# Performance work log

Hardware: AMD Instinct MI355X
Metric: run time of the kernel (lower is better)

## Reference

```python
import jax, jax.numpy as jnp
import numpy as np

GROUPS = 32
EPS = 1e-5

def group_norm(x, scale, bias):
    b, c, h, w = x.shape
    xg = x.reshape(b, GROUPS, c // GROUPS, h, w)
    mean = xg.mean(axis=(2, 3, 4), keepdims=True)
    var = xg.var(axis=(2, 3, 4), keepdims=True)
    xg = (xg - mean) * jax.lax.rsqrt(var + EPS)
    x = xg.reshape(b, c, h, w)
    return x * scale[None, :, None, None] + bias[None, :, None, None]

def conv2d(x, w, b, pad):
    y = jax.lax.conv_general_dilated(
        x, w, window_strides=(1, 1), padding=[(pad, pad), (pad, pad)],
        dimension_numbers=('NCHW', 'OIHW', 'NCHW'))
    return y + b[None, :, None, None]

def setup_inputs() -> dict:
    key = jax.random.key(0)
    ks = jax.random.split(key, 16)
    B, Cin, Cout, H, W, TDIM, NCON = 4, 128, 128, 64, 64, 512, 4
    s = 0.05
    return {
        'x': jax.random.normal(ks[0], (B, Cin, H, W), jnp.float32),
        't': jax.random.normal(ks[1], (B, TDIM), jnp.float32),
        'aim': jax.random.randint(ks[2], (B,), 0, NCON),
        'cond': jax.random.normal(ks[3], (B, Cin, H, W), jnp.float32),
        'gn1_scale': jnp.ones((Cin,), jnp.float32),
        'gn1_bias': jnp.zeros((Cin,), jnp.float32),
        'conv1_w': jax.random.normal(ks[4], (Cout, Cin, 3, 3), jnp.float32) * s,
        'conv1_b': jnp.zeros((Cout,), jnp.float32),
        'mlp_w': jax.random.normal(ks[5], (Cout, TDIM), jnp.float32) * s,
        'mlp_b': jnp.zeros((Cout,), jnp.float32),
        'cond_w': jax.random.normal(ks[6], (Cout, Cin, 1, 1), jnp.float32) * s,
        'cond_b': jnp.zeros((Cout,), jnp.float32),
        'gn2_scale': jnp.ones((Cout,), jnp.float32),
        'gn2_bias': jnp.zeros((Cout,), jnp.float32),
        'conv2_w': jax.random.normal(ks[7], (Cout, Cout, 3, 3), jnp.float32) * s,
        'conv2_b': jnp.zeros((Cout,), jnp.float32),
        'contrast_embed': jax.random.normal(ks[8], (NCON, Cout, 1, 1), jnp.float32),
    }

def reference(x, t, aim, cond, gn1_scale, gn1_bias, conv1_w, conv1_b,
              mlp_w, mlp_b, cond_w, cond_b, gn2_scale, gn2_bias,
              conv2_w, conv2_b, contrast_embed):
    # block1: GN -> SiLU -> 3x3 conv
    h = conv2d(jax.nn.silu(group_norm(x, gn1_scale, gn1_bias)), conv1_w, conv1_b, 1)
    # time embedding: SiLU -> Linear, broadcast over spatial
    temb = jax.nn.silu(t) @ mlp_w.T + mlp_b  # (b, out_ch)
    h = h + temb[:, :, None, None]
    # spatial cross-attention with cond
    c = conv2d(cond, cond_w, cond_b, 0)  # 1x1 projection, (b, C, u, v)
    C = h.shape[1]
    score = jnp.einsum('bchw,bcuv->bhwuv', h, c)  # (b, h, w, u, v)
    # NOTE: softmax over dim=1 (the spatial h axis), as in the source
    score = jax.nn.softmax(score / jnp.sqrt(jnp.float32(C)), axis=1)
    h = h + jnp.einsum('bhwuv,bcuv->bchw', score, c)
    # contrast embedding lookup
    h = h + contrast_embed[aim]  # (b, C, 1, 1) broadcast
    # block2: GN -> SiLU -> (dropout=identity at eval) -> 3x3 conv
    h = conv2d(jax.nn.silu(group_norm(h, gn2_scale, gn2_bias)), conv2_w, conv2_b, 1)
    # res_conv is Identity since in_ch == out_ch
    return h + x
```

## Files before the change

### kernel.cpp

```cpp
#include <hip/hip_runtime.h>
#include <cmath>

#define BB 4
#define CC 128
#define HH 64
#define WW 64
#define SP 4096
#define NG 32
#define TT 64
#define NS 4
#define PSZ ((size_t)BB * SP * CC)

typedef __bf16 bf16x8 __attribute__((ext_vector_type(8)));
typedef __bf16 bf16x4 __attribute__((ext_vector_type(4)));
typedef float  f32x4  __attribute__((ext_vector_type(4)));

__device__ __forceinline__ float silu_f(float v) {
    return v / (1.f + __expf(-v));
}

__global__ __launch_bounds__(256) void prep_kernel(
    const float* __restrict__ x, const float* __restrict__ gn1s,
    const float* __restrict__ gn1b, __bf16* __restrict__ aT,
    const float* __restrict__ c1w, const float* __restrict__ c2w,
    __bf16* __restrict__ wt,
    const float* __restrict__ t, const float* __restrict__ mlpw,
    const float* __restrict__ mlpb, float* __restrict__ tembw,
    const float* __restrict__ cond, const float* __restrict__ cw,
    const float* __restrict__ cb, __bf16* __restrict__ cmT,
    __bf16* __restrict__ cm2)
{
    __shared__ __align__(16) char pool[65536];
    __shared__ float rs[4], rs2[4], mean_s, inv_s;
    const int blk = blockIdx.x;
    const int tid = threadIdx.x;

    if (blk < 128) {
        const int b = blk >> 5, g = blk & 31;
        float* X = (float*)pool;
        const float* p = x + (size_t)blk * 16384;
        float s = 0.f, s2 = 0.f;
        for (int it = 0; it < 16; ++it) {
            int q = it * 256 + tid;
            float4 v = *(const float4*)&p[q * 4];
            *(float4*)&X[q * 4] = v;
            s += v.x + v.y + v.z + v.w;
            s2 += v.x * v.x + v.y * v.y + v.z * v.z + v.w * v.w;
        }
        #pragma unroll
        for (int off = 32; off >= 1; off >>= 1) {
            s  += __shfl_down(s,  off, 64);
            s2 += __shfl_down(s2, off, 64);
        }
        const int wid = tid >> 6;
        if ((tid & 63) == 0) { rs[wid] = s; rs2[wid] = s2; }
        __syncthreads();
        if (tid == 0) {
            float S = rs[0] + rs[1] + rs[2] + rs[3];
            float S2 = rs2[0] + rs2[1] + rs2[2] + rs2[3];
            float m = S * (1.f / 16384.f);
            float var = S2 * (1.f / 16384.f) - m * m;
            mean_s = m;
            inv_s = rsqrtf(var + 1e-5f);
        }
        __syncthreads();
        const float m = mean_s, inv = inv_s;
        float sc[4], bi[4];
        #pragma unroll
        for (int j = 0; j < 4; ++j) { sc[j] = gn1s[g * 4 + j]; bi[j] = gn1b[g * 4 + j]; }
        for (int it = 0; it < 16; ++it) {
            int pp = it * 256 + tid;
            bf16x4 o;
            #pragma unroll
            for (int j = 0; j < 4; ++j)
                o[j] = (__bf16)silu_f((X[j * 4096 + pp] - m) * inv * sc[j] + bi[j]);
            *(bf16x4*)&aT[((size_t)(b * SP + pp)) * CC + g * 4] = o;
        }
    } else if (blk < 146) {
        const int idx = blk - 128;
        const int wsel = idx / 9, tap = idx % 9;
        const float* src = wsel ? c2w : c1w;
        __bf16* dst = wt + (size_t)wsel * 9 * 16384 + (size_t)tap * 16384;
        for (int it = 0; it < 64; ++it) {
            int q = it * 256 + tid;
            dst[q] = (__bf16)src[(size_t)q * 9 + tap];
        }
    } else if (blk < 154) {
        const int cog = blk - 146;
        float* st = (float*)pool;
        float* wr = (float*)(pool + 8192);
        for (int it = 0; it < 8; ++it) {
            int q = it * 256 + tid;
            st[q] = silu_f(t[q]);
        }
        for (int it = 0; it < 8; ++it) {
            int q = it * 256 + tid;
            int row = q >> 7, col4 = q & 127;
            *(float4*)&wr[row * 512 + col4 * 4] =
                *(const float4*)&mlpw[(size_t)(cog * 16 + row) * 512 + col4 * 4];
        }
        __syncthreads();
        const int col = tid >> 4, seg = tid & 15;
        float acc[4] = {0.f, 0.f, 0.f, 0.f};
        for (int k = seg * 32; k < seg * 32 + 32; ++k) {
            float wv = wr[col * 512 + k];
            acc[0] += st[0 * 512 + k] * wv;
            acc[1] += st[1 * 512 + k] * wv;
            acc[2] += st[2 * 512 + k] * wv;
            acc[3] += st[3 * 512 + k] * wv;
        }
        #pragma unroll
        for (int o = 1; o < 16; o <<= 1) {
            #pragma unroll
            for (int b4 = 0; b4 < 4; ++b4)
                acc[b4] += __shfl_xor(acc[b4], o, 64);
        }
        if (seg == 0) {
            float bv = mlpb[cog * 16 + col];
            #pragma unroll
            for (int b4 = 0; b4 < 4; ++b4)
                tembw[b4 * 128 + cog * 16 + col] = acc[b4] + bv;
        }
    } else {
        const int pblk = blk - 154;
        const int b = pblk >> 6;
        const int p0 = (pblk & 63) * 64;
        const int l = tid & 63, wv = tid >> 6;
        const int l15 = l & 15, l4 = l >> 4;
        const int mB = wv * 32;

        __bf16* XT = (__bf16*)pool;
        __bf16* wl = (__bf16*)(pool + 17152);

        for (int it = 0; it < 32; ++it) {
            int q = it * 256 + tid;
            float v = cond[((size_t)(b * CC + (q >> 6))) * SP + p0 + (q & 63)];
            XT[(q & 63) * 134 + (q >> 6)] = (__bf16)v;
        }
        for (int it = 0; it < 64; ++it) {
            int q = it * 256 + tid;
            wl[(q >> 7) * 134 + (q & 127)] = (__bf16)cw[q];
        }
        __syncthreads();

        f32x4 acc[2][4];
        #pragma unroll
        for (int mb = 0; mb < 2; ++mb)
            #pragma unroll
            for (int nt = 0; nt < 4; ++nt) acc[mb][nt] = (f32x4){0.f, 0.f, 0.f, 0.f};

        #pragma unroll
        for (int ks = 0; ks < 4; ++ks) {
            bf16x8 bfr[4];
            #pragma unroll
            for (int nt = 0; nt < 4; ++nt)
                bfr[nt] = *(const bf16x8*)&XT[(nt * 16 + l15) * 134 + ks * 32 + l4 * 8];
            #pragma unroll
            for (int mb = 0; mb < 2; ++mb) {
                bf16x8 afr = *(const bf16x8*)&wl[(mB + mb * 16 + l15) * 134 + ks * 32 + l4 * 8];
                #pragma unroll
                for (int nt = 0; nt < 4; ++nt)
                    acc[mb][nt] = __builtin_amdgcn_mfma_f32_16x16x32_bf16(afr, bfr[nt], acc[mb][nt], 0, 0, 0);
            }
        }

        const float scl = 0.088388347648318447f;
        #pragma unroll
        for (int mb = 0; mb < 2; ++mb) {
            int co0 = mB + mb * 16 + l4 * 4;
            float bv[4];
            #pragma unroll
            for (int r = 0; r < 4; ++r) bv[r] = cb[co0 + r];
            #pragma unroll
            for (int nt = 0; nt < 4; ++nt) {
                int p = p0 + nt * 16 + l15;
                bf16x4 o;
                #pragma unroll
                for (int r = 0; r < 4; ++r)
                    o[r] = (__bf16)((acc[mb][nt][r] + bv[r]) * scl);
                *(bf16x4*)&cmT[((size_t)(b * SP + p)) * CC + co0] = o;
            }
        }
        __syncthreads();
        __bf16* O2 = wl;
        #pragma unroll
        for (int mb = 0; mb < 2; ++mb) {
            int co0 = mB + mb * 16 + l4 * 4;
            #pragma unroll
            for (int r = 0; r < 4; ++r) {
                float bv = cb[co0 + r];
                #pragma unroll
                for (int nt = 0; nt < 4; ++nt)
                    O2[(co0 + r) * 72 + nt * 16 + l15] = (__bf16)(acc[mb][nt][r] + bv);
            }
        }
        __syncthreads();
        #pragma unroll
        for (int it = 0; it < 4; ++it) {
            int q = it * 256 + tid;
            int co = q >> 3, pc = q & 7;
            *(bf16x8*)&cm2[((size_t)(b * CC + co)) * SP + p0 + pc * 8] =
                *(const bf16x8*)&O2[co * 72 + pc * 8];
        }
    }
}

template<bool FUSE_TEMB, bool OUT_CF>
__global__ __launch_bounds__(256, 3) void conv_mfma_kernel(
    const __bf16* __restrict__ inT, const __bf16* __restrict__ wt,
    const float* __restrict__ bias, const float* __restrict__ temb,
    const float* __restrict__ resid, __bf16* __restrict__ outT,
    float* __restrict__ outF)
{
    const int y   = blockIdx.x >> 1;
    const int coh = blockIdx.x & 1;
    const int b   = blockIdx.y;
    const int tid = threadIdx.x;
    const int l = tid & 63, wv = tid >> 6;
    const int l15 = l & 15, l4 = l >> 4;
    const int mB = (wv & 1) * 32;
    const int xh = (wv >> 1) * 32;

    __shared__ __bf16 inS[3 * 66 * 136];

    const __bf16* inTb = inT + (size_t)b * SP * CC;
    for (int q = tid; q < 3 * 66 * 16; q += 256) {
        int cc = q & 15;
        int xs = (q >> 4) % 66;
        int r  = (q >> 4) / 66;
        int yy = y + r - 1;
        int xg = xs - 1;
        bf16x8 v;
        if (((unsigned)yy < 64u) && ((unsigned)xg < 64u)) {
            v = *(const bf16x8*)&inTb[((size_t)(yy * 64 + xg)) * CC + cc * 8];
        } else {
            #pragma unroll
            for (int j = 0; j < 8; ++j) v[j] = (__bf16)0.f;
        }
        *(bf16x8*)&inS[(r * 66 + xs) * 136 + cc * 8] = v;
    }
    __syncthreads();

    f32x4 acc[2][2];
    #pragma unroll
    for (int mb = 0; mb < 2; ++mb)
        #pragma unroll
        for (int nb = 0; nb < 2; ++nb) acc[mb][nb] = (f32x4){0.f, 0.f, 0.f, 0.f};

    const __bf16* wp0 = wt + (size_t)(coh * 64 + mB + l15) * 128 + l4 * 8;
    const __bf16* wp1 = wt + (size_t)(coh * 64 + mB + 16 + l15) * 128 + l4 * 8;

    bf16x8 wb[2][2][4];
    #pragma unroll
    for (int ks = 0; ks < 4; ++ks) {
        wb[0][0][ks] = *(const bf16x8*)(wp0 + ks * 32);
        wb[0][1][ks] = *(const bf16x8*)(wp1 + ks * 32);
    }

    #pragma unroll
    for (int tap = 0; tap < 9; ++tap) {
        const int cur = tap & 1, nxt = cur ^ 1;
        if (tap < 8) {
            #pragma unroll
            for (int ks = 0; ks < 4; ++ks) {
                wb[nxt][0][ks] = *(const bf16x8*)(wp0 + (tap + 1) * 16384 + ks * 32);
                wb[nxt][1][ks] = *(const bf16x8*)(wp1 + (tap + 1) * 16384 + ks * 32);
            }
        }
        const __bf16* rb = &inS[((tap / 3) * 66 + xh + (tap % 3)) * 136];
        #pragma unroll
        for (int ks = 0; ks < 4; ++ks) {
            bf16x8 b0 = *(const bf16x8*)&rb[(l15) * 136 + ks * 32 + l4 * 8];
            bf16x8 b1 = *(const bf16x8*)&rb[(16 + l15) * 136 + ks * 32 + l4 * 8];
            acc[0][0] = __builtin_amdgcn_mfma_f32_16x16x32_bf16(wb[cur][0][ks], b0, acc[0][0], 0, 0, 0);
            acc[1][0] = __builtin_amdgcn_mfma_f32_16x16x32_bf16(wb[cur][1][ks], b0, acc[1][0], 0, 0, 0);
            acc[0][1] = __builtin_amdgcn_mfma_f32_16x16x32_bf16(wb[cur][0][ks], b1, acc[0][1], 0, 0, 0);
            acc[1][1] = __builtin_amdgcn_mfma_f32_16x16x32_bf16(wb[cur][1][ks], b1, acc[1][1], 0, 0, 0);
        }
    }

    if (OUT_CF) {
        #pragma unroll
        for (int mb = 0; mb < 2; ++mb) {
            #pragma unroll
            for (int r = 0; r < 4; ++r) {
                int co = coh * 64 + mB + mb * 16 + l4 * 4 + r;
                float bv = bias[co];
                #pragma unroll
                for (int nb = 0; nb < 2; ++nb) {
                    int p = y * 64 + xh + nb * 16 + l15;
                    size_t o = ((size_t)(b * CC + co)) * SP + p;
                    outF[o] = acc[mb][nb][r] + bv + resid[o];
                }
            }
        }
    } else {
        #pragma unroll
        for (int mb = 0; mb < 2; ++mb) {
            int co0 = coh * 64 + mB + mb * 16 + l4 * 4;
            float bv[4];
            #pragma unroll
            for (int r = 0; r < 4; ++r)
                bv[r] = bias[co0 + r] + (FUSE_TEMB ? temb[b * CC + co0 + r] : 0.f);
            #pragma unroll
            for (int nb = 0; nb < 2; ++nb) {
                int p = y * 64 + xh + nb * 16 + l15;
                bf16x4 o;
                #pragma unroll
                for (int r = 0; r < 4; ++r)
                    o[r] = (__bf16)(acc[mb][nb][r] + bv[r]);
                *(bf16x4*)&outT[((size_t)(b * SP + p)) * CC + co0] = o;
            }
        }
    }
}

#define CT2 72
#define PBS 72
#define POOL_BYTES 46080

__global__ __launch_bounds__(256, 3) void attn_kernel(
    const __bf16* __restrict__ h1T, const __bf16* __restrict__ cmT,
    const __bf16* __restrict__ cm2, __bf16* __restrict__ parts)
{
    const int w = blockIdx.x;
    const int b = blockIdx.y;
    const int s = blockIdx.z;
    const int tid = threadIdx.x;
    const int wl = tid >> 6;
    const int l = tid & 63, l15 = l & 15, l4 = l >> 4;
    const int hB = (wl & 1) * 32;
    const int cB = (wl >> 1) * 64;

    __shared__ __align__(16) char pool[POOL_BYTES];
    __bf16* ct2p = (__bf16*)pool;
    __bf16* Pb   = (__bf16*)(pool + 36864);
    __bf16* Otr  = (__bf16*)pool;

    const __bf16* h1Tb = h1T + (size_t)b * SP * CC;
    const __bf16* cmTb = cmT + (size_t)b * SP * CC;
    const __bf16* cm2b = cm2 + (size_t)b * CC * SP;

    bf16x8 hfr[4][4];
    #pragma unroll
    for (int nt = 0; nt < 4; ++nt)
        #pragma unroll
        for (int ks = 0; ks < 4; ++ks)
            hfr[nt][ks] = *(const bf16x8*)&h1Tb[((size_t)((nt * 16 + l15) * WW + w)) * CC + ks * 32 + l4 * 8];

    f32x4 acc2[2][4];
    #pragma unroll
    for (int mb = 0; mb < 2; ++mb)
        #pragma unroll
        for (int nt = 0; nt < 4; ++nt) acc2[mb][nt] = (f32x4){0.f, 0.f, 0.f, 0.f};

    const int sc = tid >> 3;
    const int stc = tid & 7;

    {
        const int uv0 = s * TT;
        #pragma unroll
        for (int it = 0; it < 4; ++it) {
            int c = it * 32 + sc;
            *(bf16x8*)&ct2p[c * CT2 + stc * 8] =
                *(const bf16x8*)&cm2b[(size_t)c * SP + uv0 + stc * 8];
        }
        const __bf16* arow = cmTb + (size_t)(uv0 + 16 * wl + l15) * CC;
        bf16x8 afr[4];
        #pragma unroll
        for (int ks = 0; ks < 4; ++ks) afr[ks] = *(const bf16x8*)&arow[ks * 32 + l4 * 8];
        f32x4 s1[4];
        #pragma unroll
        for (int nt = 0; nt < 4; ++nt) {
            s1[nt] = (f32x4){0.f, 0.f, 0.f, 0.f};
            #pragma unroll
            for (int ks = 0; ks < 4; ++ks)
                s1[nt] = __builtin_amdgcn_mfma_f32_16x16x32_bf16(afr[ks], hfr[nt][ks], s1[nt], 0, 0, 0);
        }
        #pragma unroll
        for (int r = 0; r < 4; ++r) {
            float e0 = __expf(s1[0][r]), e1 = __expf(s1[1][r]);
            float e2 = __expf(s1[2][r]), e3 = __expf(s1[3][r]);
            float sm = e0 + e1 + e2 + e3;
            sm += __shfl_xor(sm, 1, 64);
            sm += __shfl_xor(sm, 2, 64);
            sm += __shfl_xor(sm, 4, 64);
            sm += __shfl_xor(sm, 8, 64);
            float ri = 1.f / sm;
            s1[0][r] = e0 * ri; s1[1][r] = e1 * ri;
            s1[2][r] = e2 * ri; s1[3][r] = e3 * ri;
        }
        #pragma unroll
        for (int nt = 0; nt < 4; ++nt) {
            bf16x4 pk;
            pk[0] = (__bf16)s1[nt][0]; pk[1] = (__bf16)s1[nt][1];
            pk[2] = (__bf16)s1[nt][2]; pk[3] = (__bf16)s1[nt][3];
            *(bf16x4*)&Pb[(nt * 16 + l15) * PBS + 16 * wl + l4 * 4] = pk;
        }
    }

    for (int i = 0; i < SP / TT / NS; ++i) {
        const int cur = i & 1;
        __syncthreads();
        bf16x8 st4[4];
        bf16x8 afr[4];
        if (i < SP / TT / NS - 1) {
            const int uv0n = ((i + 1) * NS + s) * TT;
            #pragma unroll
            for (int it = 0; it < 4; ++it) {
                int c = it * 32 + sc;
                st4[it] = *(const bf16x8*)&cm2b[(size_t)c * SP + uv0n + stc * 8];
            }
            const __bf16* arow = cmTb + (size_t)(uv0n + 16 * wl + l15) * CC;
            #pragma unroll
            for (int ks = 0; ks < 4; ++ks) afr[ks] = *(const bf16x8*)&arow[ks * 32 + l4 * 8];
        }
        bf16x8 pfr[2][2];
        #pragma unroll
        for (int mb = 0; mb < 2; ++mb)
            #pragma unroll
            for (int ks = 0; ks < 2; ++ks)
                pfr[mb][ks] = *(const bf16x8*)&Pb[(hB + mb * 16 + l15) * PBS + ks * 32 + l4 * 8];
        __syncthreads();
        {
            const __bf16* ctR = ct2p + cur * 9216;
            #pragma unroll
            for (int mb = 0; mb < 2; ++mb)
                #pragma unroll
                for (int nt = 0; nt < 4; ++nt)
                    #pragma unroll
                    for (int ks = 0; ks < 2; ++ks) {
                        bf16x8 bfr = *(const bf16x8*)&ctR[(cB + nt * 16 + l15) * CT2 + ks * 32 + l4 * 8];
                        acc2[mb][nt] = __builtin_amdgcn_mfma_f32_16x16x32_bf16(
                            pfr[mb][ks], bfr, acc2[mb][nt], 0, 0, 0);
                    }
        }
        if (i < SP / TT / NS - 1) {
            __bf16* ctW = ct2p + (cur ^ 1) * 9216;
            #pragma unroll
            for (int it = 0; it < 4; ++it) {
                int c = it * 32 + sc;
                *(bf16x8*)&ctW[c * CT2 + stc * 8] = st4[it];
            }
            f32x4 s1[4];
            #pragma unroll
            for (int nt = 0; nt < 4; ++nt) {
                s1[nt] = (f32x4){0.f, 0.f, 0.f, 0.f};
                #pragma unroll
                for (int ks = 0; ks < 4; ++ks)
                    s1[nt] = __builtin_amdgcn_mfma_f32_16x16x32_bf16(afr[ks], hfr[nt][ks], s1[nt], 0, 0, 0);
            }
            #pragma unroll
            for (int r = 0; r < 4; ++r) {
                float e0 = __expf(s1[0][r]), e1 = __expf(s1[1][r]);
                float e2 = __expf(s1[2][r]), e3 = __expf(s1[3][r]);
                float sm = e0 + e1 + e2 + e3;
                sm += __shfl_xor(sm, 1, 64);
                sm += __shfl_xor(sm, 2, 64);
                sm += __shfl_xor(sm, 4, 64);
                sm += __shfl_xor(sm, 8, 64);
                float ri = 1.f / sm;
                s1[0][r] = e0 * ri; s1[1][r] = e1 * ri;
                s1[2][r] = e2 * ri; s1[3][r] = e3 * ri;
            }
            #pragma unroll
            for (int nt = 0; nt < 4; ++nt) {
                bf16x4 pk;
                pk[0] = (__bf16)s1[nt][0]; pk[1] = (__bf16)s1[nt][1];
                pk[2] = (__bf16)s1[nt][2]; pk[3] = (__bf16)s1[nt][3];
                *(bf16x4*)&Pb[(nt * 16 + l15) * PBS + 16 * wl + l4 * 4] = pk;
            }
        }
    }

    __syncthreads();
    #pragma unroll
    for (int mb = 0; mb < 2; ++mb)
        #pragma unroll
        for (int nt = 0; nt < 4; ++nt)
            #pragma unroll
            for (int r = 0; r < 4; ++r)
                Otr[(hB + mb * 16 + l4 * 4 + r) * 136 + cB + nt * 16 + l15] =
                    (__bf16)acc2[mb][nt][r];
    __syncthreads();
    __bf16* pO = parts + (size_t)s * PSZ;
    #pragma unroll
    for (int it = 0; it < 4; ++it) {
        int q = it * 256 + tid;
        int h = q >> 4, cc = q & 15;
        *(bf16x8*)&pO[((size_t)(b * SP + h * WW + w)) * CC + cc * 8] =
            *(const bf16x8*)&Otr[h * 136 + cc * 8];
    }
}

__global__ __launch_bounds__(256) void gn2_stats_kernel(
    const __bf16* __restrict__ h1T, const __bf16* __restrict__ parts,
    const int* __restrict__ aim, const float* __restrict__ emb,
    float* __restrict__ pstat)
{
    const int pb = blockIdx.x, b = blockIdx.y;
    const int tid = threadIdx.x;
    const int c4 = tid & 31;
    const float4 ev = *(const float4*)&emb[aim[b] * CC + c4 * 4];
    float s = 0.f, s2 = 0.f;
    for (int it = 0; it < 8; ++it) {
        int prow = it * 8 + (tid >> 5);
        size_t base = ((size_t)(b * SP + pb * 64 + prow)) * CC + c4 * 4;
        bf16x4 hv = *(const bf16x4*)&h1T[base];
        float v0 = (float)hv[0] + ev.x;
        float v1 = (float)hv[1] + ev.y;
        float v2 = (float)hv[2] + ev.z;
        float v3 = (float)hv[3] + ev.w;
        #pragma unroll
        for (int k = 0; k < NS; ++k) {
            bf16x4 a = *(const bf16x4*)&parts[(size_t)k * PSZ + base];
            v0 += (float)a[0]; v1 += (float)a[1];
            v2 += (float)a[2]; v3 += (float)a[3];
        }
        s += v0 + v1 + v2 + v3;
        s2 += v0 * v0 + v1 * v1 + v2 * v2 + v3 * v3;
    }
    s  += __shfl_down(s,  32, 64);
    s2 += __shfl_down(s2, 32, 64);
    __shared__ float ls[4][32][2];
    const int wv = tid >> 6, ll = tid & 63;
    if (ll < 32) { ls[wv][ll][0] = s; ls[wv][ll][1] = s2; }
    __syncthreads();
    if (tid < 32) {
        float S = ls[0][tid][0] + ls[1][tid][0] + ls[2][tid][0] + ls[3][tid][0];
        float S2 = ls[0][tid][1] + ls[1][tid][1] + ls[2][tid][1] + ls[3][tid][1];
        int g = tid;
        pstat[(((size_t)b * NG + g) * 64 + pb) * 2]     = S;
        pstat[(((size_t)b * NG + g) * 64 + pb) * 2 + 1] = S2;
    }
}

__global__ __launch_bounds__(256) void gn2_apply_kernel(
    const __bf16* __restrict__ h1T, const __bf16* __restrict__ parts,
    const int* __restrict__ aim, const float* __restrict__ emb,
    const float* __restrict__ pstat, const float* __restrict__ scale,
    const float* __restrict__ bias, __bf16* __restrict__ outT)
{
    const int pb = blockIdx.x, b = blockIdx.y;
    const int tid = threadIdx.x;
    const int c4 = tid & 31;
    const int g = c4;
    __shared__ float st[32][2];
    if (tid < 32) {
        float S = 0.f, S2 = 0.f;
        const float* ps = pstat + ((size_t)b * NG + tid) * 128;
        for (int k = 0; k < 64; ++k) { S += ps[k * 2]; S2 += ps[k * 2 + 1]; }
        float mm = S * (1.f / 16384.f);
        float var = S2 * (1.f / 16384.f) - mm * mm;
        st[tid][0] = mm;
        st[tid][1] = rsqrtf(var + 1e-5f);
    }
    __syncthreads();
    const float4 ev = *(const float4*)&emb[aim[b] * CC + c4 * 4];
    const float4 sc = *(const float4*)&scale[c4 * 4];
    const float4 bi = *(const float4*)&bias[c4 * 4];
    const float m = st[g][0], inv = st[g][1];
    for (int it = 0; it < 8; ++it) {
        int prow = it * 8 + (tid >> 5);
        size_t base = ((size_t)(b * SP + pb * 64 + prow)) * CC + c4 * 4;
        bf16x4 hv = *(const bf16x4*)&h1T[base];
        float v0 = (float)hv[0] + ev.x;
        float v1 = (float)hv[1] + ev.y;
        float v2 = (float)hv[2] + ev.z;
        float v3 = (float)hv[3] + ev.w;
        #pragma unroll
        for (int k = 0; k < NS; ++k) {
            bf16x4 a = *(const bf16x4*)&parts[(size_t)k * PSZ + base];
            v0 += (float)a[0]; v1 += (float)a[1];
            v2 += (float)a[2]; v3 += (float)a[3];
        }
        bf16x4 o;
        o[0] = (__bf16)silu_f((v0 - m) * inv * sc.x + bi.x);
        o[1] = (__bf16)silu_f((v1 - m) * inv * sc.y + bi.y);
        o[2] = (__bf16)silu_f((v2 - m) * inv * sc.z + bi.z);
        o[3] = (__bf16)silu_f((v3 - m) * inv * sc.w + bi.w);
        *(bf16x4*)&outT[base] = o;
    }
}

extern "C" void kernel_launch(void* const* d_in, const int* in_sizes, int n_in,
                              void* d_out, int out_size, void* d_ws, size_t ws_size,
                              hipStream_t stream)
{
    const float* x     = (const float*)d_in[0];
    const float* t     = (const float*)d_in[1];
    const int*   aim   = (const int*)  d_in[2];
    const float* cond  = (const float*)d_in[3];
    const float* gn1s  = (const float*)d_in[4];
    const float* gn1b  = (const float*)d_in[5];
    const float* c1w   = (const float*)d_in[6];
    const float* c1b   = (const float*)d_in[7];
    const float* mlpw  = (const float*)d_in[8];
    const float* mlpb  = (const float*)d_in[9];
    const float* cw    = (const float*)d_in[10];
    const float* cb    = (const float*)d_in[11];
    const float* gn2s  = (const float*)d_in[12];
    const float* gn2b  = (const float*)d_in[13];
    const float* c2w   = (const float*)d_in[14];
    const float* c2b   = (const float*)d_in[15];
    const float* emb   = (const float*)d_in[16];
    float* out = (float*)d_out;
    float* ws = (float*)d_ws;

    __bf16* aT    = (__bf16*)ws;
    __bf16* h1T   = (__bf16*)(ws + 1048576);
    __bf16* cmT   = (__bf16*)(ws + 2097152);
    __bf16* cm2   = (__bf16*)(ws + 3145728);
    __bf16* parts = (__bf16*)(ws + 4194304);
    __bf16* wt    = (__bf16*)(ws + 8388608);
    float*  tembw = ws + 8536064;
    float*  pstat = ws + 8536576;

    prep_kernel<<<dim3(410), dim3(256), 0, stream>>>(
        x, gn1s, gn1b, aT, c1w, c2w, wt, t, mlpw, mlpb, tembw,
        cond, cw, cb, cmT, cm2);
    conv_mfma_kernel<true, false><<<dim3(128, BB), dim3(256), 0, stream>>>(
        aT, wt, c1b, tembw, nullptr, h1T, nullptr);
    attn_kernel<<<dim3(WW, BB, NS), dim3(256), 0, stream>>>(h1T, cmT, cm2, parts);
    gn2_stats_kernel<<<dim3(64, BB), dim3(256), 0, stream>>>(h1T, parts, aim, emb, pstat);
    gn2_apply_kernel<<<dim3(64, BB), dim3(256), 0, stream>>>(
        h1T, parts, aim, emb, pstat, gn2s, gn2b, aT);
    conv_mfma_kernel<false, true><<<dim3(128, BB), dim3(256), 0, stream>>>(
        aT, wt + (size_t)9 * 16384, c2b, nullptr, x, nullptr, out);
}
```

Before: 243.3 us.

## Retile conv to half-row blocks, halve attention splits, materialize pre-GN2 activations

The conv kernel now uses blocks that cover half an output row and 64 output channels, with one 16-channel tile per wave, a channel-blocked shared layout and occupancy hint 4, which doubles the grid. Attention split count drops from 4 to 2. GN2 stats now writes the summed pre-norm activation so the apply pass reads one buffer instead of re-summing the partials. The prep kernel drops its shared-memory staging of x, the MLP weights and the 1x1 conv weights and reads them directly from global memory, cutting LDS use. Together these aim to raise occupancy and cut redundant memory traffic, at the cost of reloading weights per wave.

```diff
diff --git a/kernel.cpp b/kernel.cpp
--- a/kernel.cpp
+++ b/kernel.cpp
@@ -8,7 +8,7 @@
 #define SP 4096
 #define NG 32
 #define TT 64
-#define NS 4
+#define NS 2
 #define PSZ ((size_t)BB * SP * CC)
 
 typedef __bf16 bf16x8 __attribute__((ext_vector_type(8)));
@@ -30,20 +30,18 @@
     const float* __restrict__ cb, __bf16* __restrict__ cmT,
     __bf16* __restrict__ cm2)
 {
-    __shared__ __align__(16) char pool[65536];
+    __shared__ __align__(16) char pool[18432];
     __shared__ float rs[4], rs2[4], mean_s, inv_s;
     const int blk = blockIdx.x;
     const int tid = threadIdx.x;
 
     if (blk < 128) {
         const int b = blk >> 5, g = blk & 31;
-        float* X = (float*)pool;
         const float* p = x + (size_t)blk * 16384;
         float s = 0.f, s2 = 0.f;
         for (int it = 0; it < 16; ++it) {
             int q = it * 256 + tid;
             float4 v = *(const float4*)&p[q * 4];
-            *(float4*)&X[q * 4] = v;
             s += v.x + v.y + v.z + v.w;
             s2 += v.x * v.x + v.y * v.y + v.z * v.z + v.w * v.w;
         }
@@ -73,7 +71,7 @@
             bf16x4 o;
             #pragma unroll
             for (int j = 0; j < 4; ++j)
-                o[j] = (__bf16)silu_f((X[j * 4096 + pp] - m) * inv * sc[j] + bi[j]);
+                o[j] = (__bf16)silu_f((p[j * 4096 + pp] - m) * inv * sc[j] + bi[j]);
             *(bf16x4*)&aT[((size_t)(b * SP + pp)) * CC + g * 4] = o;
         }
     } else if (blk < 146) {
@@ -88,26 +86,26 @@
     } else if (blk < 154) {
         const int cog = blk - 146;
         float* st = (float*)pool;
-        float* wr = (float*)(pool + 8192);
         for (int it = 0; it < 8; ++it) {
             int q = it * 256 + tid;
             st[q] = silu_f(t[q]);
         }
-        for (int it = 0; it < 8; ++it) {
-            int q = it * 256 + tid;
-            int row = q >> 7, col4 = q & 127;
-            *(float4*)&wr[row * 512 + col4 * 4] =
-                *(const float4*)&mlpw[(size_t)(cog * 16 + row) * 512 + col4 * 4];
-        }
         __syncthreads();
         const int col = tid >> 4, seg = tid & 15;
+        const float* wr = mlpw + (size_t)(cog * 16 + col) * 512 + seg * 32;
         float acc[4] = {0.f, 0.f, 0.f, 0.f};
-        for (int k = seg * 32; k < seg * 32 + 32; ++k) {
-            float wv = wr[col * 512 + k];
-            acc[0] += st[0 * 512 + k] * wv;
-            acc[1] += st[1 * 512 + k] * wv;
-            acc[2] += st[2 * 512 + k] * wv;
-            acc[3] += st[3 * 512 + k] * wv;
+        #pragma unroll
+        for (int k8 = 0; k8 < 8; ++k8) {
+            float4 wv = *(const float4*)&wr[k8 * 4];
+            #pragma unroll
+            for (int j = 0; j < 4; ++j) {
+                int k = seg * 32 + k8 * 4 + j;
+                float w4 = (&wv.x)[j];
+                acc[0] += st[0 * 512 + k] * w4;
+                acc[1] += st[1 * 512 + k] * w4;
+                acc[2] += st[2 * 512 + k] * w4;
+                acc[3] += st[3 * 512 + k] * w4;
+            }
         }
         #pragma unroll
         for (int o = 1; o < 16; o <<= 1) {
@@ -130,16 +128,11 @@
         const int mB = wv * 32;
 
         __bf16* XT = (__bf16*)pool;
-        __bf16* wl = (__bf16*)(pool + 17152);
 
         for (int it = 0; it < 32; ++it) {
             int q = it * 256 + tid;
             float v = cond[((size_t)(b * CC + (q >> 6))) * SP + p0 + (q & 63)];
-            XT[(q & 63) * 134 + (q >> 6)] = (__bf16)v;
-        }
-        for (int it = 0; it < 64; ++it) {
-            int q = it * 256 + tid;
-            wl[(q >> 7) * 134 + (q & 127)] = (__bf16)cw[q];
+            XT[(q & 63) * 136 + (q >> 6)] = (__bf16)v;
         }
         __syncthreads();
 
@@ -154,10 +147,17 @@
             bf16x8 bfr[4];
             #pragma unroll
             for (int nt = 0; nt < 4; ++nt)
-                bfr[nt] = *(const bf16x8*)&XT[(nt * 16 + l15) * 134 + ks * 32 + l4 * 8];
+                bfr[nt] = *(const bf16x8*)&XT[(nt * 16 + l15) * 136 + ks * 32 + l4 * 8];
             #pragma unroll
             for (int mb = 0; mb < 2; ++mb) {
-                bf16x8 afr = *(const bf16x8*)&wl[(mB + mb * 16 + l15) * 134 + ks * 32 + l4 * 8];
+                const float* wrow = cw + (size_t)(mB + mb * 16 + l15) * 128 + ks * 32 + l4 * 8;
+                float4 wa = *(const float4*)wrow;
+                float4 wb4 = *(const float4*)(wrow + 4);
+                bf16x8 afr;
+                afr[0] = (__bf16)wa.x; afr[1] = (__bf16)wa.y;
+                afr[2] = (__bf16)wa.z; afr[3] = (__bf16)wa.w;
+                afr[4] = (__bf16)wb4.x; afr[5] = (__bf16)wb4.y;
+                afr[6] = (__bf16)wb4.z; afr[7] = (__bf16)wb4.w;
                 #pragma unroll
                 for (int nt = 0; nt < 4; ++nt)
                     acc[mb][nt] = __builtin_amdgcn_mfma_f32_16x16x32_bf16(afr, bfr[nt], acc[mb][nt], 0, 0, 0);
@@ -182,7 +182,7 @@
             }
         }
         __syncthreads();
-        __bf16* O2 = wl;
+        __bf16* O2 = (__bf16*)pool;
         #pragma unroll
         for (int mb = 0; mb < 2; ++mb) {
             int co0 = mB + mb * 16 + l4 * 4;
@@ -206,30 +206,32 @@
 }
 
 template<bool FUSE_TEMB, bool OUT_CF>
-__global__ __launch_bounds__(256, 3) void conv_mfma_kernel(
+__global__ __launch_bounds__(256, 4) void conv_mfma_kernel(
     const __bf16* __restrict__ inT, const __bf16* __restrict__ wt,
     const float* __restrict__ bias, const float* __restrict__ temb,
     const float* __restrict__ resid, __bf16* __restrict__ outT,
     float* __restrict__ outF)
 {
-    const int y   = blockIdx.x >> 1;
+    const int y   = blockIdx.x >> 2;
+    const int xh2 = (blockIdx.x >> 1) & 1;
     const int coh = blockIdx.x & 1;
+    const int x0  = xh2 * 32;
     const int b   = blockIdx.y;
     const int tid = threadIdx.x;
     const int l = tid & 63, wv = tid >> 6;
     const int l15 = l & 15, l4 = l >> 4;
-    const int mB = (wv & 1) * 32;
-    const int xh = (wv >> 1) * 32;
-
-    __shared__ __bf16 inS[3 * 66 * 136];
+    const int co_w = coh * 64 + wv * 16;
+
+    __shared__ __bf16 inS[3 * 16 * 34 * 8];
 
     const __bf16* inTb = inT + (size_t)b * SP * CC;
-    for (int q = tid; q < 3 * 66 * 16; q += 256) {
+    for (int q = tid; q < 3 * 34 * 16; q += 256) {
         int cc = q & 15;
-        int xs = (q >> 4) % 66;
-        int r  = (q >> 4) / 66;
+        int t2 = q >> 4;
+        int xs = t2 % 34;
+        int r  = t2 / 34;
         int yy = y + r - 1;
-        int xg = xs - 1;
+        int xg = x0 + xs - 1;
         bf16x8 v;
         if (((unsigned)yy < 64u) && ((unsigned)xg < 64u)) {
             v = *(const bf16x8*)&inTb[((size_t)(yy * 64 + xg)) * CC + cc * 8];
@@ -237,80 +239,65 @@
             #pragma unroll
             for (int j = 0; j < 8; ++j) v[j] = (__bf16)0.f;
         }
-        *(bf16x8*)&inS[(r * 66 + xs) * 136 + cc * 8] = v;
+        *(bf16x8*)&inS[((r * 16 + cc) * 34 + xs) * 8] = v;
     }
     __syncthreads();
 
-    f32x4 acc[2][2];
+    f32x4 acc[2];
+    acc[0] = (f32x4){0.f, 0.f, 0.f, 0.f};
+    acc[1] = (f32x4){0.f, 0.f, 0.f, 0.f};
+
+    const __bf16* wp = wt + (size_t)(co_w + l15) * 128 + l4 * 8;
+    bf16x8 wb[2][4];
     #pragma unroll
-    for (int mb = 0; mb < 2; ++mb)
-        #pragma unroll
-        for (int nb = 0; nb < 2; ++nb) acc[mb][nb] = (f32x4){0.f, 0.f, 0.f, 0.f};
-
-    const __bf16* wp0 = wt + (size_t)(coh * 64 + mB + l15) * 128 + l4 * 8;
-    const __bf16* wp1 = wt + (size_t)(coh * 64 + mB + 16 + l15) * 128 + l4 * 8;
-
-    bf16x8 wb[2][2][4];
-    #pragma unroll
-    for (int ks = 0; ks < 4; ++ks) {
-        wb[0][0][ks] = *(const bf16x8*)(wp0 + ks * 32);
-        wb[0][1][ks] = *(const bf16x8*)(wp1 + ks * 32);
-    }
+    for (int ks = 0; ks < 4; ++ks)
+        wb[0][ks] = *(const bf16x8*)(wp + ks * 32);
 
     #pragma unroll
     for (int tap = 0; tap < 9; ++tap) {
         const int cur = tap & 1, nxt = cur ^ 1;
         if (tap < 8) {
             #pragma unroll
-            for (int ks = 0; ks < 4; ++ks) {
-                wb[nxt][0][ks] = *(const bf16x8*)(wp0 + (tap + 1) * 16384 + ks * 32);
-                wb[nxt][1][ks] = *(const bf16x8*)(wp1 + (tap + 1) * 16384 + ks * 32);
-            }
-        }
-        const __bf16* rb = &inS[((tap / 3) * 66 + xh + (tap % 3)) * 136];
+            for (int ks = 0; ks < 4; ++ks)
+                wb[nxt][ks] = *(const bf16x8*)(wp + (tap + 1) * 16384 + ks * 32);
+        }
+        const int rr = tap / 3, dx = tap % 3;
         #pragma unroll
         for (int ks = 0; ks < 4; ++ks) {
-            bf16x8 b0 = *(const bf16x8*)&rb[(l15) * 136 + ks * 32 + l4 * 8];
-            bf16x8 b1 = *(const bf16x8*)&rb[(16 + l15) * 136 + ks * 32 + l4 * 8];
-            acc[0][0] = __builtin_amdgcn_mfma_f32_16x16x32_bf16(wb[cur][0][ks], b0, acc[0][0], 0, 0, 0);
-            acc[1][0] = __builtin_amdgcn_mfma_f32_16x16x32_bf16(wb[cur][1][ks], b0, acc[1][0], 0, 0, 0);
-            acc[0][1] = __builtin_amdgcn_mfma_f32_16x16x32_bf16(wb[cur][0][ks], b1, acc[0][1], 0, 0, 0);
-            acc[1][1] = __builtin_amdgcn_mfma_f32_16x16x32_bf16(wb[cur][1][ks], b1, acc[1][1], 0, 0, 0);
+            const __bf16* rb = &inS[((rr * 16 + ks * 4 + l4) * 34) * 8];
+            bf16x8 b0 = *(const bf16x8*)&rb[(dx + l15) * 8];
+            bf16x8 b1 = *(const bf16x8*)&rb[(16 + dx + l15) * 8];
+            acc[0] = __builtin_amdgcn_mfma_f32_16x16x32_bf16(wb[cur][ks], b0, acc[0], 0, 0, 0);
+            acc[1] = __builtin_amdgcn_mfma_f32_16x16x32_bf16(wb[cur][ks], b1, acc[1], 0, 0, 0);
         }
     }
 
     if (OUT_CF) {
         #pragma unroll
-        for (int mb = 0; mb < 2; ++mb) {
-            #pragma unroll
-            for (int r = 0; r < 4; ++r) {
-                int co = coh * 64 + mB + mb * 16 + l4 * 4 + r;
-                float bv = bias[co];
-                #pragma unroll
-                for (int nb = 0; nb < 2; ++nb) {
-                    int p = y * 64 + xh + nb * 16 + l15;
-                    size_t o = ((size_t)(b * CC + co)) * SP + p;
-                    outF[o] = acc[mb][nb][r] + bv + resid[o];
-                }
+        for (int r = 0; r < 4; ++r) {
+            int co = co_w + l4 * 4 + r;
+            float bv = bias[co];
+            #pragma unroll
+            for (int nb = 0; nb < 2; ++nb) {
+                int p = y * 64 + x0 + nb * 16 + l15;
+                size_t o = ((size_t)(b * CC + co)) * SP + p;
+                outF[o] = acc[nb][r] + bv + resid[o];
             }
         }
     } else {
-        #pragma unroll
-        for (int mb = 0; mb < 2; ++mb) {
-            int co0 = coh * 64 + mB + mb * 16 + l4 * 4;
-            float bv[4];
+        int co0 = co_w + l4 * 4;
+        float bv[4];
+        #pragma unroll
+        for (int r = 0; r < 4; ++r)
+            bv[r] = bias[co0 + r] + (FUSE_TEMB ? temb[b * CC + co0 + r] : 0.f);
+        #pragma unroll
+        for (int nb = 0; nb < 2; ++nb) {
+            int p = y * 64 + x0 + nb * 16 + l15;
+            bf16x4 o;
             #pragma unroll
             for (int r = 0; r < 4; ++r)
-                bv[r] = bias[co0 + r] + (FUSE_TEMB ? temb[b * CC + co0 + r] : 0.f);
-            #pragma unroll
-            for (int nb = 0; nb < 2; ++nb) {
-                int p = y * 64 + xh + nb * 16 + l15;
-                bf16x4 o;
-                #pragma unroll
-                for (int r = 0; r < 4; ++r)
-                    o[r] = (__bf16)(acc[mb][nb][r] + bv[r]);
-                *(bf16x4*)&outT[((size_t)(b * SP + p)) * CC + co0] = o;
-            }
+                o[r] = (__bf16)(acc[nb][r] + bv[r]);
+            *(bf16x4*)&outT[((size_t)(b * SP + p)) * CC + co0] = o;
         }
     }
 }
@@ -496,7 +483,7 @@
 __global__ __launch_bounds__(256) void gn2_stats_kernel(
     const __bf16* __restrict__ h1T, const __bf16* __restrict__ parts,
     const int* __restrict__ aim, const float* __restrict__ emb,
-    float* __restrict__ pstat)
+    __bf16* __restrict__ h2T, float* __restrict__ pstat)
 {
     const int pb = blockIdx.x, b = blockIdx.y;
     const int tid = threadIdx.x;
@@ -517,6 +504,10 @@
             v0 += (float)a[0]; v1 += (float)a[1];
             v2 += (float)a[2]; v3 += (float)a[3];
         }
+        bf16x4 o;
+        o[0] = (__bf16)v0; o[1] = (__bf16)v1;
+        o[2] = (__bf16)v2; o[3] = (__bf16)v3;
+        *(bf16x4*)&h2T[base] = o;
         s += v0 + v1 + v2 + v3;
         s2 += v0 * v0 + v1 * v1 + v2 * v2 + v3 * v3;
     }
@@ -536,10 +527,9 @@
 }
 
 __global__ __launch_bounds__(256) void gn2_apply_kernel(
-    const __bf16* __restrict__ h1T, const __bf16* __restrict__ parts,
-    const int* __restrict__ aim, const float* __restrict__ emb,
-    const float* __restrict__ pstat, const float* __restrict__ scale,
-    const float* __restrict__ bias, __bf16* __restrict__ outT)
+    const __bf16* __restrict__ h2T, const float* __restrict__ pstat,
+    const float* __restrict__ scale, const float* __restrict__ bias,
+    __bf16* __restrict__ outT)
 {
     const int pb = blockIdx.x, b = blockIdx.y;
     const int tid = threadIdx.x;
@@ -556,29 +546,18 @@
         st[tid][1] = rsqrtf(var + 1e-5f);
     }
     __syncthreads();
-    const float4 ev = *(const float4*)&emb[aim[b] * CC + c4 * 4];
     const float4 sc = *(const float4*)&scale[c4 * 4];
     const float4 bi = *(const float4*)&bias[c4 * 4];
     const float m = st[g][0], inv = st[g][1];
     for (int it = 0; it < 8; ++it) {
         int prow = it * 8 + (tid >> 5);
         size_t base = ((size_t)(b * SP + pb * 64 + prow)) * CC + c4 * 4;
-        bf16x4 hv = *(const bf16x4*)&h1T[base];
-        float v0 = (float)hv[0] + ev.x;
-        float v1 = (float)hv[1] + ev.y;
-        float v2 = (float)hv[2] + ev.z;
-        float v3 = (float)hv[3] + ev.w;
-        #pragma unroll
-        for (int k = 0; k < NS; ++k) {
-            bf16x4 a = *(const bf16x4*)&parts[(size_t)k * PSZ + base];
-            v0 += (float)a[0]; v1 += (float)a[1];
-            v2 += (float)a[2]; v3 += (float)a[3];
-        }
+        bf16x4 hv = *(const bf16x4*)&h2T[base];
         bf16x4 o;
-        o[0] = (__bf16)silu_f((v0 - m) * inv * sc.x + bi.x);
-        o[1] = (__bf16)silu_f((v1 - m) * inv * sc.y + bi.y);
-        o[2] = (__bf16)silu_f((v2 - m) * inv * sc.z + bi.z);
-        o[3] = (__bf16)silu_f((v3 - m) * inv * sc.w + bi.w);
+        o[0] = (__bf16)silu_f(((float)hv[0] - m) * inv * sc.x + bi.x);
+        o[1] = (__bf16)silu_f(((float)hv[1] - m) * inv * sc.y + bi.y);
+        o[2] = (__bf16)silu_f(((float)hv[2] - m) * inv * sc.z + bi.z);
+        o[3] = (__bf16)silu_f(((float)hv[3] - m) * inv * sc.w + bi.w);
         *(bf16x4*)&outT[base] = o;
     }
 }
@@ -612,19 +591,19 @@
     __bf16* cmT   = (__bf16*)(ws + 2097152);
     __bf16* cm2   = (__bf16*)(ws + 3145728);
     __bf16* parts = (__bf16*)(ws + 4194304);
-    __bf16* wt    = (__bf16*)(ws + 8388608);
-    float*  tembw = ws + 8536064;
-    float*  pstat = ws + 8536576;
+    __bf16* wt    = (__bf16*)(ws + 6291456);
+    float*  tembw = ws + 6438912;
+    float*  pstat = ws + 6439424;
+    __bf16* h2T   = cmT;
 
     prep_kernel<<<dim3(410), dim3(256), 0, stream>>>(
         x, gn1s, gn1b, aT, c1w, c2w, wt, t, mlpw, mlpb, tembw,
         cond, cw, cb, cmT, cm2);
-    conv_mfma_kernel<true, false><<<dim3(128, BB), dim3(256), 0, stream>>>(
+    conv_mfma_kernel<true, false><<<dim3(256, BB), dim3(256), 0, stream>>>(
         aT, wt, c1b, tembw, nullptr, h1T, nullptr);
     attn_kernel<<<dim3(WW, BB, NS), dim3(256), 0, stream>>>(h1T, cmT, cm2, parts);
-    gn2_stats_kernel<<<dim3(64, BB), dim3(256), 0, stream>>>(h1T, parts, aim, emb, pstat);
-    gn2_apply_kernel<<<dim3(64, BB), dim3(256), 0, stream>>>(
-        h1T, parts, aim, emb, pstat, gn2s, gn2b, aT);
-    conv_mfma_kernel<false, true><<<dim3(128, BB), dim3(256), 0, stream>>>(
+    gn2_stats_kernel<<<dim3(64, BB), dim3(256), 0, stream>>>(h1T, parts, aim, emb, h2T, pstat);
+    gn2_apply_kernel<<<dim3(64, BB), dim3(256), 0, stream>>>(h2T, pstat, gn2s, gn2b, aT);
+    conv_mfma_kernel<false, true><<<dim3(256, BB), dim3(256), 0, stream>>>(
         aT, wt + (size_t)9 * 16384, c2b, nullptr, x, nullptr, out);
 }
```

Result: faster. 229.8 us (-5.5%).
